# Kernel tuning notes

Measured on AMD Instinct MI355X. Metric: run time of the kernel, lower is better.

## Reference

```python
import jax, jax.numpy as jnp
import numpy as np

NUM_CODES = 100000
DIM = 64
N = 65536   # B*T flattened visits
L = 48      # max codes per visit (padded with -1)
C = 1.0     # Poincare ball curvature
MIN_NORM = 1e-15
BALL_EPS = 1e-5   # geoopt projx boundary eps for float32
ATANH_EPS = 1e-7  # clamp artanh argument below 1


def _projx(x):
    # Poincare ball projection: pull points with norm >= (1-eps)/sqrt(c) back inside.
    sqrt_c = jnp.sqrt(C)
    norm = jnp.maximum(jnp.linalg.norm(x, axis=-1, keepdims=True), MIN_NORM)
    maxnorm = (1.0 - BALL_EPS) / sqrt_c
    return jnp.where(norm > maxnorm, x * (maxnorm / norm), x)


def setup_inputs() -> dict:
    key = jax.random.key(0)
    k1, k2, k3 = jax.random.split(key, 3)
    emb = jax.random.normal(k1, (NUM_CODES, DIM), dtype=jnp.float32) * 0.001
    emb = _projx(emb)
    ids = jax.random.randint(k2, (N, L), 0, NUM_CODES)
    pad = jax.random.uniform(k3, (N, L)) < 0.3
    code_ids = jnp.where(pad, jnp.int64(-1) if jax.config.jax_enable_x64 else -1, ids)
    return {"code_ids": code_ids, "emb": emb}


def reference(code_ids, emb):
    # code_ids: [N, L] int, -1 = padding; emb: [NUM_CODES, DIM] Poincare points.
    sqrt_c = jnp.sqrt(jnp.asarray(C, emb.dtype))
    mask = code_ids >= 0                               # [N, L]
    safe_ids = jnp.where(mask, code_ids, 0)
    x = emb[safe_ids]                                  # [N, L, D] gather
    # logmap0: artanh(sqrt(c)*||x||) * x / (sqrt(c)*||x||)
    norm = jnp.maximum(jnp.linalg.norm(x, axis=-1, keepdims=True), MIN_NORM)
    arg = jnp.minimum(sqrt_c * norm, 1.0 - ATANH_EPS)
    tangents = (jnp.arctanh(arg) / (sqrt_c * norm)) * x  # [N, L, D]
    m = mask[..., None].astype(emb.dtype)
    s = jnp.sum(tangents * m, axis=1)                  # [N, D]
    cnt = jnp.sum(m, axis=1)                           # [N, 1]
    return s / jnp.maximum(cnt, 1.0)                   # zeros for empty visits
```

## Files before the change

kernel.cpp:

```cpp
#include <hip/hip_runtime.h>


#define LCODES 48
#define DIM 64

__global__ __launch_bounds__(256)
void amax_kernel(const float* __restrict__ emb, unsigned* __restrict__ bmax,
                 long n4) {
    const uint4* __restrict__ u4 = reinterpret_cast<const uint4*>(emb);
    unsigned m = 0;
    for (long i = (long)blockIdx.x * 256 + threadIdx.x; i < n4; i += 256L * 256L) {
        const uint4 w = u4[i];
        m = max(m, w.x & 0x7fffffffu);
        m = max(m, w.y & 0x7fffffffu);
        m = max(m, w.z & 0x7fffffffu);
        m = max(m, w.w & 0x7fffffffu);
    }
    #pragma unroll
    for (int d = 1; d <= 32; d <<= 1)
        m = max(m, (unsigned)__shfl_xor((int)m, d, 64));
    __shared__ unsigned sm[4];
    if ((threadIdx.x & 63) == 0) sm[threadIdx.x >> 6] = m;
    __syncthreads();
    if (threadIdx.x == 0)
        bmax[blockIdx.x] = max(max(sm[0], sm[1]), max(sm[2], sm[3]));
}

__device__ __forceinline__ float global_amax(const unsigned* __restrict__ bmax) {
    const int lane = threadIdx.x & 63;
    unsigned m = max(max(bmax[lane], bmax[lane + 64]),
                     max(bmax[lane + 128], bmax[lane + 192]));
    #pragma unroll
    for (int d = 1; d <= 32; d <<= 1)
        m = max(m, (unsigned)__shfl_xor((int)m, d, 64));
    return __uint_as_float(m);
}

__global__ __launch_bounds__(256)
void build_i8_kernel(const float* __restrict__ emb,
                     const unsigned* __restrict__ bmax,
                     unsigned char* __restrict__ tab,
                     float* __restrict__ qsout, int C) {
    const float amax = global_amax(bmax);
    const float qs   = amax * (1.0006f / 127.f);
    const float invq = (amax > 0.f) ? (127.f / (amax * 1.0006f)) : 0.f;
    if (blockIdx.x == 0 && threadIdx.x == 0) qsout[0] = qs;

    const int tid  = threadIdx.x;
    const int lane = tid & 63;
    const int wave = tid >> 6;
    const int g = lane >> 3;
    const int s = lane & 7;
    const int r = blockIdx.x * 32 + wave * 8 + g;
    if (r >= C) return;

    const float4* __restrict__ emb4 = reinterpret_cast<const float4*>(emb);
    const float4 a = emb4[r * 16 + 2 * s];
    const float4 b = emb4[r * 16 + 2 * s + 1];

    float ss = a.x*a.x + a.y*a.y + a.z*a.z + a.w*a.w
             + b.x*b.x + b.y*b.y + b.z*b.z + b.w*b.w;
    ss += __shfl_xor(ss, 1, 64);
    ss += __shfl_xor(ss, 2, 64);
    ss += __shfl_xor(ss, 4, 64);

    float scale;
    if (__builtin_expect(ss > 0.04f, 0)) {
        const float norm = fmaxf(sqrtf(ss), 1e-15f);
        const float arg  = fminf(norm, 1.f - 1e-7f);
        scale = 0.5f * logf((1.f + arg) / (1.f - arg)) / norm;
    } else {
        scale = 1.f + ss * (0.33333333333f + ss * (0.2f + ss * 0.14285714285f));
    }
    scale *= invq;

    const float t[8] = { a.x*scale, a.y*scale, a.z*scale, a.w*scale,
                         b.x*scale, b.y*scale, b.z*scale, b.w*scale };
    unsigned u[8];
    #pragma unroll
    for (int k = 0; k < 8; ++k)
        u[k] = (unsigned)((int)rintf(t[k]) + 128);

    uint2 w;
    w.x = u[0] | (u[1] << 8) | (u[2] << 16) | (u[3] << 24);
    w.y = u[4] | (u[5] << 8) | (u[6] << 16) | (u[7] << 24);
    reinterpret_cast<uint2*>(tab)[r * 8 + s] = w;
}

__global__ __launch_bounds__(256)
void visit_gather_i8_kernel(const int* __restrict__ ids,
                            const unsigned char* __restrict__ tab,
                            const float* __restrict__ qsp,
                            float* __restrict__ out, int N) {
    const float qs = qsp[0];

    const int tid  = threadIdx.x;
    const int lane = tid & 63;
    const int wave = tid >> 6;
    const int v    = blockIdx.x * 4 + wave;
    if (v >= N) return;

    int myid = -1;
    if (lane < LCODES) myid = ids[(long)v * LCODES + lane];

    const unsigned long long valid = __ballot(myid >= 0);
    const float cnt = (float)__popcll(valid);

    const int g = lane >> 3;
    const int s = lane & 7;

    const uint2* __restrict__ tab2 = reinterpret_cast<const uint2*>(tab);

    float4 accA = make_float4(0.f, 0.f, 0.f, 0.f);
    float4 accB = make_float4(0.f, 0.f, 0.f, 0.f);

    #pragma unroll
    for (int it = 0; it < LCODES / 8; ++it) {
        const int id     = __shfl(myid, it * 8 + g, 64);
        const float keep = (id >= 0) ? 1.f : 0.f;
        const unsigned base = ((unsigned)(id >= 0 ? id : 0)) << 3;

        const uint2 w = tab2[base + s];

        accA.x += (float)( w.x        & 0xff) * keep;
        accA.y += (float)((w.x >>  8) & 0xff) * keep;
        accA.z += (float)((w.x >> 16) & 0xff) * keep;
        accA.w += (float)( w.x >> 24        ) * keep;
        accB.x += (float)( w.y        & 0xff) * keep;
        accB.y += (float)((w.y >>  8) & 0xff) * keep;
        accB.z += (float)((w.y >> 16) & 0xff) * keep;
        accB.w += (float)( w.y >> 24        ) * keep;
    }

    #pragma unroll
    for (int d = 8; d <= 32; d <<= 1) {
        accA.x += __shfl_xor(accA.x, d, 64);
        accA.y += __shfl_xor(accA.y, d, 64);
        accA.z += __shfl_xor(accA.z, d, 64);
        accA.w += __shfl_xor(accA.w, d, 64);
        accB.x += __shfl_xor(accB.x, d, 64);
        accB.y += __shfl_xor(accB.y, d, 64);
        accB.z += __shfl_xor(accB.z, d, 64);
        accB.w += __shfl_xor(accB.w, d, 64);
    }

    if (lane < 8) {
        const float inv  = 1.f / fmaxf(cnt, 1.f);
        const float bias = 128.f * cnt;
        float4 rA = make_float4(qs * (accA.x - bias) * inv, qs * (accA.y - bias) * inv,
                                qs * (accA.z - bias) * inv, qs * (accA.w - bias) * inv);
        float4 rB = make_float4(qs * (accB.x - bias) * inv, qs * (accB.y - bias) * inv,
                                qs * (accB.z - bias) * inv, qs * (accB.w - bias) * inv);
        float4* o = reinterpret_cast<float4*>(out) + (long)v * (DIM / 4);
        o[2 * s]     = rA;
        o[2 * s + 1] = rB;
    }
}

__global__ __launch_bounds__(256, 4)
void visit_fp32_kernel(const int* __restrict__ ids,
                       const float* __restrict__ emb,
                       float* __restrict__ out, int N) {
    const int tid  = threadIdx.x;
    const int lane = tid & 63;
    const int wave = tid >> 6;
    const int v    = blockIdx.x * 4 + wave;
    if (v >= N) return;

    int myid = -1;
    if (lane < LCODES) myid = ids[(long)v * LCODES + lane];
    const unsigned long long valid = __ballot(myid >= 0);
    const float cnt = (float)__popcll(valid);
    const int g = lane >> 3, s = lane & 7;
    const float4* __restrict__ emb4 = reinterpret_cast<const float4*>(emb);
    float4 accA = make_float4(0.f,0.f,0.f,0.f), accB = make_float4(0.f,0.f,0.f,0.f);
    #pragma unroll
    for (int it = 0; it < LCODES / 8; ++it) {
        const int id = __shfl(myid, it * 8 + g, 64);
        const float keep = (id >= 0) ? 1.f : 0.f;
        const unsigned base = ((unsigned)(id >= 0 ? id : 0)) << 4;
        float4 a = emb4[base + s], b = emb4[base + 8 + s];
        float ss = a.x*a.x + a.y*a.y + a.z*a.z + a.w*a.w
                 + b.x*b.x + b.y*b.y + b.z*b.z + b.w*b.w;
        ss += __shfl_xor(ss, 1, 64);
        ss += __shfl_xor(ss, 2, 64);
        ss += __shfl_xor(ss, 4, 64);
        float scale;
        if (__builtin_expect(__any(ss > 0.04f), 0)) {
            const float norm = fmaxf(sqrtf(ss), 1e-15f);
            const float arg  = fminf(norm, 1.f - 1e-7f);
            scale = 0.5f * logf((1.f + arg) / (1.f - arg)) / norm;
        } else {
            scale = 1.f + ss * (0.33333333333f + ss * (0.2f + ss * 0.14285714285f));
        }
        scale *= keep;
        accA.x += a.x*scale; accA.y += a.y*scale; accA.z += a.z*scale; accA.w += a.w*scale;
        accB.x += b.x*scale; accB.y += b.y*scale; accB.z += b.z*scale; accB.w += b.w*scale;
    }
    #pragma unroll
    for (int d = 8; d <= 32; d <<= 1) {
        accA.x += __shfl_xor(accA.x, d, 64); accA.y += __shfl_xor(accA.y, d, 64);
        accA.z += __shfl_xor(accA.z, d, 64); accA.w += __shfl_xor(accA.w, d, 64);
        accB.x += __shfl_xor(accB.x, d, 64); accB.y += __shfl_xor(accB.y, d, 64);
        accB.z += __shfl_xor(accB.z, d, 64); accB.w += __shfl_xor(accB.w, d, 64);
    }
    if (lane < 8) {
        const float inv = 1.f / fmaxf(cnt, 1.f);
        float4* o = reinterpret_cast<float4*>(out) + (long)v * (DIM / 4);
        o[2*s]   = make_float4(accA.x*inv, accA.y*inv, accA.z*inv, accA.w*inv);
        o[2*s+1] = make_float4(accB.x*inv, accB.y*inv, accB.z*inv, accB.w*inv);
    }
}

extern "C" void kernel_launch(void* const* d_in, const int* in_sizes, int n_in,
                              void* d_out, int out_size, void* d_ws, size_t ws_size,
                              hipStream_t stream) {
    const int*   ids = (const int*)d_in[0];
    const float* emb = (const float*)d_in[1];
    float*       out = (float*)d_out;

    const int N = in_sizes[0] / LCODES;
    const int C = in_sizes[1] / DIM;

    const size_t tab_off = 4096;
    const size_t need = tab_off + (size_t)C * DIM;

    if (ws_size >= need) {
        unsigned*      bmax = (unsigned*)d_ws;
        float*         qsp  = (float*)((char*)d_ws + 1024);
        unsigned char* tab  = (unsigned char*)d_ws + tab_off;

        const long n4 = (long)C * DIM / 4;
        hipLaunchKernelGGL(amax_kernel, dim3(256), dim3(256), 0, stream,
                           emb, bmax, n4);
        const int blocksA = (C + 31) / 32;
        hipLaunchKernelGGL(build_i8_kernel, dim3(blocksA), dim3(256), 0, stream,
                           emb, bmax, tab, qsp, C);
        const int blocksB = (N + 3) / 4;
        hipLaunchKernelGGL(visit_gather_i8_kernel, dim3(blocksB), dim3(256), 0, stream,
                           ids, tab, qsp, out, N);
    } else {
        const int blocks = (N + 3) / 4;
        hipLaunchKernelGGL(visit_fp32_kernel, dim3(blocks), dim3(256), 0, stream,
                           ids, emb, out, N);
    }
}
```

Measured before the change: 110.8 us.

## Fuse amax, int8 table build and gather into one cooperative kernel

Replaces the three-kernel sequence (amax reduction, int8 table build, visit gather) with a single cooperative grid-stride kernel of 2048 blocks that uses grid.sync between phases. This removes two kernel launch gaps. The gather accumulation also switches from per-byte float adds to packed 16-bit integer SIMD-within-a-register adds on the masked words, which cuts the ALU work per loaded word. Costs are the grid-wide barriers, a fixed grid size that may limit occupancy during the gather phase, and a fallback to the old path if the cooperative launch fails.

New measurement: 426.3 us. 285% more time.

```diff
diff --git a/kernel.cpp b/kernel.cpp
--- a/kernel.cpp
+++ b/kernel.cpp
@@ -1,8 +1,162 @@
 #include <hip/hip_runtime.h>
+#include <hip/hip_cooperative_groups.h>
+
+namespace cg = cooperative_groups;
 
 
 #define LCODES 48
 #define DIM 64
+#define NBLK 2048
+#define NTHR 256
+
+__global__ __launch_bounds__(NTHR, 8)
+void fused_kernel(const int* __restrict__ ids,
+                  const float* __restrict__ emb,
+                  unsigned char* __restrict__ tab,
+                  unsigned* __restrict__ bmax,
+                  float* __restrict__ out,
+                  int N, int C) {
+    cg::grid_group grid = cg::this_grid();
+    const int tid  = threadIdx.x;
+    const int lane = tid & 63;
+    const int wave = tid >> 6;
+    const int bid  = blockIdx.x;
+
+    __shared__ unsigned sm[4];
+
+    {
+        const long n4 = (long)C * DIM / 4;
+        const uint4* __restrict__ u4 = reinterpret_cast<const uint4*>(emb);
+        unsigned m = 0;
+        for (long i = (long)bid * NTHR + tid; i < n4; i += (long)NBLK * NTHR) {
+            const uint4 w = u4[i];
+            m = max(m, w.x & 0x7fffffffu);
+            m = max(m, w.y & 0x7fffffffu);
+            m = max(m, w.z & 0x7fffffffu);
+            m = max(m, w.w & 0x7fffffffu);
+        }
+        #pragma unroll
+        for (int d = 1; d <= 32; d <<= 1)
+            m = max(m, (unsigned)__shfl_xor((int)m, d, 64));
+        if (lane == 0) sm[wave] = m;
+        __syncthreads();
+        if (tid == 0) bmax[bid] = max(max(sm[0], sm[1]), max(sm[2], sm[3]));
+    }
+    grid.sync();
+
+    float qs, invq;
+    {
+        unsigned gm = 0;
+        for (int i = tid; i < NBLK; i += NTHR) gm = max(gm, bmax[i]);
+        #pragma unroll
+        for (int d = 1; d <= 32; d <<= 1)
+            gm = max(gm, (unsigned)__shfl_xor((int)gm, d, 64));
+        __syncthreads();
+        if (lane == 0) sm[wave] = gm;
+        __syncthreads();
+        const unsigned g0 = max(max(sm[0], sm[1]), max(sm[2], sm[3]));
+        const float amax = __uint_as_float(g0);
+        qs   = amax * (1.0006f / 127.f);
+        invq = (amax > 0.f) ? (127.f / (amax * 1.0006f)) : 0.f;
+    }
+    {
+        const int g = lane >> 3;
+        const int s = lane & 7;
+        const float4* __restrict__ emb4 = reinterpret_cast<const float4*>(emb);
+        for (int rb = bid * 32; rb < C; rb += NBLK * 32) {
+            const int r = rb + wave * 8 + g;
+            if (r < C) {
+                const float4 a = emb4[r * 16 + 2 * s];
+                const float4 b = emb4[r * 16 + 2 * s + 1];
+
+                float ss = a.x*a.x + a.y*a.y + a.z*a.z + a.w*a.w
+                         + b.x*b.x + b.y*b.y + b.z*b.z + b.w*b.w;
+                ss += __shfl_xor(ss, 1, 64);
+                ss += __shfl_xor(ss, 2, 64);
+                ss += __shfl_xor(ss, 4, 64);
+
+                float scale;
+                if (__builtin_expect(ss > 0.04f, 0)) {
+                    const float norm = fmaxf(sqrtf(ss), 1e-15f);
+                    const float arg  = fminf(norm, 1.f - 1e-7f);
+                    scale = 0.5f * logf((1.f + arg) / (1.f - arg)) / norm;
+                } else {
+                    scale = 1.f + ss * (0.33333333333f + ss * (0.2f + ss * 0.14285714285f));
+                }
+                scale *= invq;
+
+                const float t[8] = { a.x*scale, a.y*scale, a.z*scale, a.w*scale,
+                                     b.x*scale, b.y*scale, b.z*scale, b.w*scale };
+                unsigned u[8];
+                #pragma unroll
+                for (int k = 0; k < 8; ++k)
+                    u[k] = (unsigned)((int)rintf(t[k]) + 128);
+
+                uint2 w;
+                w.x = u[0] | (u[1] << 8) | (u[2] << 16) | (u[3] << 24);
+                w.y = u[4] | (u[5] << 8) | (u[6] << 16) | (u[7] << 24);
+                reinterpret_cast<uint2*>(tab)[r * 8 + s] = w;
+            }
+        }
+    }
+    grid.sync();
+
+    {
+        const int g = lane >> 3;
+        const int s = lane & 7;
+        const uint2* __restrict__ tab2 = reinterpret_cast<const uint2*>(tab);
+
+        for (int v = bid * 4 + wave; v < N; v += NBLK * 4) {
+            int myid = -1;
+            if (lane < LCODES) myid = ids[(long)v * LCODES + lane];
+
+            const unsigned long long valid = __ballot(myid >= 0);
+            const float cnt = (float)__popcll(valid);
+
+            unsigned aEx = 0, aOx = 0, aEy = 0, aOy = 0;
+
+            #pragma unroll
+            for (int it = 0; it < LCODES / 8; ++it) {
+                const int id = __shfl(myid, it * 8 + g, 64);
+                const unsigned msk  = (id >= 0) ? 0xffffffffu : 0u;
+                const unsigned base = ((unsigned)(id >= 0 ? id : 0)) << 3;
+
+                uint2 w = tab2[base + s];
+                w.x &= msk;  w.y &= msk;
+
+                aEx +=  w.x       & 0x00ff00ffu;
+                aOx += (w.x >> 8) & 0x00ff00ffu;
+                aEy +=  w.y       & 0x00ff00ffu;
+                aOy += (w.y >> 8) & 0x00ff00ffu;
+            }
+
+            #pragma unroll
+            for (int d = 8; d <= 32; d <<= 1) {
+                aEx += (unsigned)__shfl_xor((int)aEx, d, 64);
+                aOx += (unsigned)__shfl_xor((int)aOx, d, 64);
+                aEy += (unsigned)__shfl_xor((int)aEy, d, 64);
+                aOy += (unsigned)__shfl_xor((int)aOy, d, 64);
+            }
+
+            if (lane < 8) {
+                const float qinv  = qs / fmaxf(cnt, 1.f);
+                const float fbias = 128.f * cnt;
+                float4 rA, rB;
+                rA.x = ((float)(aEx & 0xffffu) - fbias) * qinv;
+                rA.y = ((float)(aOx & 0xffffu) - fbias) * qinv;
+                rA.z = ((float)(aEx >> 16)     - fbias) * qinv;
+                rA.w = ((float)(aOx >> 16)     - fbias) * qinv;
+                rB.x = ((float)(aEy & 0xffffu) - fbias) * qinv;
+                rB.y = ((float)(aOy & 0xffffu) - fbias) * qinv;
+                rB.z = ((float)(aEy >> 16)     - fbias) * qinv;
+                rB.w = ((float)(aOy >> 16)     - fbias) * qinv;
+                float4* o = reinterpret_cast<float4*>(out) + (long)v * (DIM / 4);
+                o[2 * s]     = rA;
+                o[2 * s + 1] = rB;
+            }
+        }
+    }
+}
 
 __global__ __launch_bounds__(256)
 void amax_kernel(const float* __restrict__ emb, unsigned* __restrict__ bmax,
@@ -26,7 +180,7 @@
         bmax[blockIdx.x] = max(max(sm[0], sm[1]), max(sm[2], sm[3]));
 }
 
-__device__ __forceinline__ float global_amax(const unsigned* __restrict__ bmax) {
+__device__ __forceinline__ float global_amax256(const unsigned* __restrict__ bmax) {
     const int lane = threadIdx.x & 63;
     unsigned m = max(max(bmax[lane], bmax[lane + 64]),
                      max(bmax[lane + 128], bmax[lane + 192]));
@@ -41,7 +195,7 @@
                      const unsigned* __restrict__ bmax,
                      unsigned char* __restrict__ tab,
                      float* __restrict__ qsout, int C) {
-    const float amax = global_amax(bmax);
+    const float amax = global_amax256(bmax);
     const float qs   = amax * (1.0006f / 127.f);
     const float invq = (amax > 0.f) ? (127.f / (amax * 1.0006f)) : 0.f;
     if (blockIdx.x == 0 && threadIdx.x == 0) qsout[0] = qs;
@@ -49,8 +203,7 @@
     const int tid  = threadIdx.x;
     const int lane = tid & 63;
     const int wave = tid >> 6;
-    const int g = lane >> 3;
-    const int s = lane & 7;
+    const int g = lane >> 3, s = lane & 7;
     const int r = blockIdx.x * 32 + wave * 8 + g;
     if (r >= C) return;
 
@@ -93,7 +246,6 @@
                             const float* __restrict__ qsp,
                             float* __restrict__ out, int N) {
     const float qs = qsp[0];
-
     const int tid  = threadIdx.x;
     const int lane = tid & 63;
     const int wave = tid >> 6;
@@ -102,55 +254,43 @@
 
     int myid = -1;
     if (lane < LCODES) myid = ids[(long)v * LCODES + lane];
-
     const unsigned long long valid = __ballot(myid >= 0);
     const float cnt = (float)__popcll(valid);
-
-    const int g = lane >> 3;
-    const int s = lane & 7;
-
+    const int g = lane >> 3, s = lane & 7;
     const uint2* __restrict__ tab2 = reinterpret_cast<const uint2*>(tab);
 
-    float4 accA = make_float4(0.f, 0.f, 0.f, 0.f);
-    float4 accB = make_float4(0.f, 0.f, 0.f, 0.f);
-
+    unsigned aEx = 0, aOx = 0, aEy = 0, aOy = 0;
     #pragma unroll
     for (int it = 0; it < LCODES / 8; ++it) {
-        const int id     = __shfl(myid, it * 8 + g, 64);
-        const float keep = (id >= 0) ? 1.f : 0.f;
+        const int id = __shfl(myid, it * 8 + g, 64);
+        const unsigned msk  = (id >= 0) ? 0xffffffffu : 0u;
         const unsigned base = ((unsigned)(id >= 0 ? id : 0)) << 3;
-
-        const uint2 w = tab2[base + s];
-
-        accA.x += (float)( w.x        & 0xff) * keep;
-        accA.y += (float)((w.x >>  8) & 0xff) * keep;
-        accA.z += (float)((w.x >> 16) & 0xff) * keep;
-        accA.w += (float)( w.x >> 24        ) * keep;
-        accB.x += (float)( w.y        & 0xff) * keep;
-        accB.y += (float)((w.y >>  8) & 0xff) * keep;
-        accB.z += (float)((w.y >> 16) & 0xff) * keep;
-        accB.w += (float)( w.y >> 24        ) * keep;
-    }
-
+        uint2 w = tab2[base + s];
+        w.x &= msk;  w.y &= msk;
+        aEx +=  w.x       & 0x00ff00ffu;
+        aOx += (w.x >> 8) & 0x00ff00ffu;
+        aEy +=  w.y       & 0x00ff00ffu;
+        aOy += (w.y >> 8) & 0x00ff00ffu;
+    }
     #pragma unroll
     for (int d = 8; d <= 32; d <<= 1) {
-        accA.x += __shfl_xor(accA.x, d, 64);
-        accA.y += __shfl_xor(accA.y, d, 64);
-        accA.z += __shfl_xor(accA.z, d, 64);
-        accA.w += __shfl_xor(accA.w, d, 64);
-        accB.x += __shfl_xor(accB.x, d, 64);
-        accB.y += __shfl_xor(accB.y, d, 64);
-        accB.z += __shfl_xor(accB.z, d, 64);
-        accB.w += __shfl_xor(accB.w, d, 64);
-    }
-
+        aEx += (unsigned)__shfl_xor((int)aEx, d, 64);
+        aOx += (unsigned)__shfl_xor((int)aOx, d, 64);
+        aEy += (unsigned)__shfl_xor((int)aEy, d, 64);
+        aOy += (unsigned)__shfl_xor((int)aOy, d, 64);
+    }
     if (lane < 8) {
-        const float inv  = 1.f / fmaxf(cnt, 1.f);
-        const float bias = 128.f * cnt;
-        float4 rA = make_float4(qs * (accA.x - bias) * inv, qs * (accA.y - bias) * inv,
-                                qs * (accA.z - bias) * inv, qs * (accA.w - bias) * inv);
-        float4 rB = make_float4(qs * (accB.x - bias) * inv, qs * (accB.y - bias) * inv,
-                                qs * (accB.z - bias) * inv, qs * (accB.w - bias) * inv);
+        const float qinv  = qs / fmaxf(cnt, 1.f);
+        const float fbias = 128.f * cnt;
+        float4 rA, rB;
+        rA.x = ((float)(aEx & 0xffffu) - fbias) * qinv;
+        rA.y = ((float)(aOx & 0xffffu) - fbias) * qinv;
+        rA.z = ((float)(aEx >> 16)     - fbias) * qinv;
+        rA.w = ((float)(aOx >> 16)     - fbias) * qinv;
+        rB.x = ((float)(aEy & 0xffffu) - fbias) * qinv;
+        rB.y = ((float)(aOy & 0xffffu) - fbias) * qinv;
+        rB.z = ((float)(aEy >> 16)     - fbias) * qinv;
+        rB.w = ((float)(aOy >> 16)     - fbias) * qinv;
         float4* o = reinterpret_cast<float4*>(out) + (long)v * (DIM / 4);
         o[2 * s]     = rA;
         o[2 * s + 1] = rB;
@@ -222,23 +362,31 @@
     const int N = in_sizes[0] / LCODES;
     const int C = in_sizes[1] / DIM;
 
-    const size_t tab_off = 4096;
+    const size_t tab_off = 16384;
     const size_t need = tab_off + (size_t)C * DIM;
 
     if (ws_size >= need) {
         unsigned*      bmax = (unsigned*)d_ws;
-        float*         qsp  = (float*)((char*)d_ws + 1024);
+        float*         qsp  = (float*)((char*)d_ws + 8192);
         unsigned char* tab  = (unsigned char*)d_ws + tab_off;
 
-        const long n4 = (long)C * DIM / 4;
-        hipLaunchKernelGGL(amax_kernel, dim3(256), dim3(256), 0, stream,
-                           emb, bmax, n4);
-        const int blocksA = (C + 31) / 32;
-        hipLaunchKernelGGL(build_i8_kernel, dim3(blocksA), dim3(256), 0, stream,
-                           emb, bmax, tab, qsp, C);
-        const int blocksB = (N + 3) / 4;
-        hipLaunchKernelGGL(visit_gather_i8_kernel, dim3(blocksB), dim3(256), 0, stream,
-                           ids, tab, qsp, out, N);
+        int n = N, c = C;
+        void* args[] = { (void*)&ids, (void*)&emb, (void*)&tab,
+                         (void*)&bmax, (void*)&out, (void*)&n, (void*)&c };
+        hipError_t err = hipLaunchCooperativeKernel(
+            (void*)fused_kernel, dim3(NBLK), dim3(NTHR), args, 0, stream);
+
+        if (err != hipSuccess) {
+            const long n4 = (long)C * DIM / 4;
+            hipLaunchKernelGGL(amax_kernel, dim3(256), dim3(256), 0, stream,
+                               emb, bmax, n4);
+            const int blocksA = (C + 31) / 32;
+            hipLaunchKernelGGL(build_i8_kernel, dim3(blocksA), dim3(256), 0, stream,
+                               emb, bmax, tab, qsp, C);
+            const int blocksB = (N + 3) / 4;
+            hipLaunchKernelGGL(visit_gather_i8_kernel, dim3(blocksB), dim3(256), 0,
+                               stream, ids, tab, qsp, out, N);
+        }
     } else {
         const int blocks = (N + 3) / 4;
         hipLaunchKernelGGL(visit_fp32_kernel, dim3(blocks), dim3(256), 0, stream,
```

## Process two visits per wave with packed 16-bit SWAR integer accumulation

Applied to the files above, without the earlier changes.

Each wave in the gather kernel now handles two visits, so it issues twice as many independent table loads per iteration. Accumulation switches from eight float adds per load to packed-integer SWAR sums, with two byte lanes held in 16-bit halves of each register. The shuffle reduction also runs on the packed integers, roughly halving the shuffle count per visit. Headroom holds: 48 codes times 255 fits in 16 bits, but register pressure and write divergence rise somewhat.

Measured after the change: 107.9 us. 2.6% less time.

```diff
diff --git a/kernel.cpp b/kernel.cpp
--- a/kernel.cpp
+++ b/kernel.cpp
@@ -26,7 +26,7 @@
         bmax[blockIdx.x] = max(max(sm[0], sm[1]), max(sm[2], sm[3]));
 }
 
-__device__ __forceinline__ float global_amax(const unsigned* __restrict__ bmax) {
+__device__ __forceinline__ float global_amax256(const unsigned* __restrict__ bmax) {
     const int lane = threadIdx.x & 63;
     unsigned m = max(max(bmax[lane], bmax[lane + 64]),
                      max(bmax[lane + 128], bmax[lane + 192]));
@@ -41,7 +41,7 @@
                      const unsigned* __restrict__ bmax,
                      unsigned char* __restrict__ tab,
                      float* __restrict__ qsout, int C) {
-    const float amax = global_amax(bmax);
+    const float amax = global_amax256(bmax);
     const float qs   = amax * (1.0006f / 127.f);
     const float invq = (amax > 0.f) ? (127.f / (amax * 1.0006f)) : 0.f;
     if (blockIdx.x == 0 && threadIdx.x == 0) qsout[0] = qs;
@@ -49,8 +49,7 @@
     const int tid  = threadIdx.x;
     const int lane = tid & 63;
     const int wave = tid >> 6;
-    const int g = lane >> 3;
-    const int s = lane & 7;
+    const int g = lane >> 3, s = lane & 7;
     const int r = blockIdx.x * 32 + wave * 8 + g;
     if (r >= C) return;
 
@@ -88,72 +87,98 @@
 }
 
 __global__ __launch_bounds__(256)
-void visit_gather_i8_kernel(const int* __restrict__ ids,
-                            const unsigned char* __restrict__ tab,
-                            const float* __restrict__ qsp,
-                            float* __restrict__ out, int N) {
+void visit_gather_i8x2_kernel(const int* __restrict__ ids,
+                              const unsigned char* __restrict__ tab,
+                              const float* __restrict__ qsp,
+                              float* __restrict__ out, int N) {
     const float qs = qsp[0];
 
     const int tid  = threadIdx.x;
     const int lane = tid & 63;
     const int wave = tid >> 6;
-    const int v    = blockIdx.x * 4 + wave;
-    if (v >= N) return;
-
-    int myid = -1;
-    if (lane < LCODES) myid = ids[(long)v * LCODES + lane];
-
-    const unsigned long long valid = __ballot(myid >= 0);
-    const float cnt = (float)__popcll(valid);
+    const int v0   = (blockIdx.x * 4 + wave) * 2;
+    if (v0 >= N) return;
+    const bool has1 = (v0 + 1) < N;
+
+    int myid0 = -1, myid1 = -1;
+    if (lane < LCODES) {
+        myid0 = ids[(long)v0 * LCODES + lane];
+        if (has1) myid1 = ids[(long)(v0 + 1) * LCODES + lane];
+    }
+
+    const float cnt0 = (float)__popcll(__ballot(myid0 >= 0));
+    const float cnt1 = (float)__popcll(__ballot(myid1 >= 0));
 
     const int g = lane >> 3;
     const int s = lane & 7;
-
     const uint2* __restrict__ tab2 = reinterpret_cast<const uint2*>(tab);
 
-    float4 accA = make_float4(0.f, 0.f, 0.f, 0.f);
-    float4 accB = make_float4(0.f, 0.f, 0.f, 0.f);
+    unsigned aEx0 = 0, aOx0 = 0, aEy0 = 0, aOy0 = 0;
+    unsigned aEx1 = 0, aOx1 = 0, aEy1 = 0, aOy1 = 0;
 
     #pragma unroll
     for (int it = 0; it < LCODES / 8; ++it) {
-        const int id     = __shfl(myid, it * 8 + g, 64);
-        const float keep = (id >= 0) ? 1.f : 0.f;
-        const unsigned base = ((unsigned)(id >= 0 ? id : 0)) << 3;
-
-        const uint2 w = tab2[base + s];
-
-        accA.x += (float)( w.x        & 0xff) * keep;
-        accA.y += (float)((w.x >>  8) & 0xff) * keep;
-        accA.z += (float)((w.x >> 16) & 0xff) * keep;
-        accA.w += (float)( w.x >> 24        ) * keep;
-        accB.x += (float)( w.y        & 0xff) * keep;
-        accB.y += (float)((w.y >>  8) & 0xff) * keep;
-        accB.z += (float)((w.y >> 16) & 0xff) * keep;
-        accB.w += (float)( w.y >> 24        ) * keep;
+        const int j   = it * 8 + g;
+        const int id0 = __shfl(myid0, j, 64);
+        const int id1 = __shfl(myid1, j, 64);
+        const unsigned msk0  = (id0 >= 0) ? 0xffffffffu : 0u;
+        const unsigned msk1  = (id1 >= 0) ? 0xffffffffu : 0u;
+        const unsigned base0 = ((unsigned)(id0 >= 0 ? id0 : 0)) << 3;
+        const unsigned base1 = ((unsigned)(id1 >= 0 ? id1 : 0)) << 3;
+
+        uint2 w0 = tab2[base0 + s];
+        uint2 w1 = tab2[base1 + s];
+        w0.x &= msk0;  w0.y &= msk0;
+        w1.x &= msk1;  w1.y &= msk1;
+
+        aEx0 +=  w0.x       & 0x00ff00ffu;
+        aOx0 += (w0.x >> 8) & 0x00ff00ffu;
+        aEy0 +=  w0.y       & 0x00ff00ffu;
+        aOy0 += (w0.y >> 8) & 0x00ff00ffu;
+        aEx1 +=  w1.x       & 0x00ff00ffu;
+        aOx1 += (w1.x >> 8) & 0x00ff00ffu;
+        aEy1 +=  w1.y       & 0x00ff00ffu;
+        aOy1 += (w1.y >> 8) & 0x00ff00ffu;
     }
 
     #pragma unroll
     for (int d = 8; d <= 32; d <<= 1) {
-        accA.x += __shfl_xor(accA.x, d, 64);
-        accA.y += __shfl_xor(accA.y, d, 64);
-        accA.z += __shfl_xor(accA.z, d, 64);
-        accA.w += __shfl_xor(accA.w, d, 64);
-        accB.x += __shfl_xor(accB.x, d, 64);
-        accB.y += __shfl_xor(accB.y, d, 64);
-        accB.z += __shfl_xor(accB.z, d, 64);
-        accB.w += __shfl_xor(accB.w, d, 64);
-    }
-
-    if (lane < 8) {
-        const float inv  = 1.f / fmaxf(cnt, 1.f);
-        const float bias = 128.f * cnt;
-        float4 rA = make_float4(qs * (accA.x - bias) * inv, qs * (accA.y - bias) * inv,
-                                qs * (accA.z - bias) * inv, qs * (accA.w - bias) * inv);
-        float4 rB = make_float4(qs * (accB.x - bias) * inv, qs * (accB.y - bias) * inv,
-                                qs * (accB.z - bias) * inv, qs * (accB.w - bias) * inv);
-        float4* o = reinterpret_cast<float4*>(out) + (long)v * (DIM / 4);
-        o[2 * s]     = rA;
-        o[2 * s + 1] = rB;
+        aEx0 += (unsigned)__shfl_xor((int)aEx0, d, 64);
+        aOx0 += (unsigned)__shfl_xor((int)aOx0, d, 64);
+        aEy0 += (unsigned)__shfl_xor((int)aEy0, d, 64);
+        aOy0 += (unsigned)__shfl_xor((int)aOy0, d, 64);
+        aEx1 += (unsigned)__shfl_xor((int)aEx1, d, 64);
+        aOx1 += (unsigned)__shfl_xor((int)aOx1, d, 64);
+        aEy1 += (unsigned)__shfl_xor((int)aEy1, d, 64);
+        aOy1 += (unsigned)__shfl_xor((int)aOy1, d, 64);
+    }
+
+    if (lane < 16) {
+        const bool second = lane >= 8;
+        if (!second || has1) {
+            const int  ss8   = lane & 7;
+            const int  v     = v0 + (second ? 1 : 0);
+            const float cnt  = second ? cnt1 : cnt0;
+            const unsigned eX = second ? aEx1 : aEx0;
+            const unsigned oX = second ? aOx1 : aOx0;
+            const unsigned eY = second ? aEy1 : aEy0;
+            const unsigned oY = second ? aOy1 : aOy0;
+
+            const float qinv  = qs / fmaxf(cnt, 1.f);
+            const float fbias = 128.f * cnt;
+            float4 rA, rB;
+            rA.x = ((float)(eX & 0xffffu) - fbias) * qinv;
+            rA.y = ((float)(oX & 0xffffu) - fbias) * qinv;
+            rA.z = ((float)(eX >> 16)     - fbias) * qinv;
+            rA.w = ((float)(oX >> 16)     - fbias) * qinv;
+            rB.x = ((float)(eY & 0xffffu) - fbias) * qinv;
+            rB.y = ((float)(oY & 0xffffu) - fbias) * qinv;
+            rB.z = ((float)(eY >> 16)     - fbias) * qinv;
+            rB.w = ((float)(oY >> 16)     - fbias) * qinv;
+            float4* o = reinterpret_cast<float4*>(out) + (long)v * (DIM / 4);
+            o[2 * ss8]     = rA;
+            o[2 * ss8 + 1] = rB;
+        }
     }
 }
 
@@ -236,9 +261,9 @@
         const int blocksA = (C + 31) / 32;
         hipLaunchKernelGGL(build_i8_kernel, dim3(blocksA), dim3(256), 0, stream,
                            emb, bmax, tab, qsp, C);
-        const int blocksB = (N + 3) / 4;
-        hipLaunchKernelGGL(visit_gather_i8_kernel, dim3(blocksB), dim3(256), 0, stream,
-                           ids, tab, qsp, out, N);
+        const int blocksB = (N + 7) / 8;
+        hipLaunchKernelGGL(visit_gather_i8x2_kernel, dim3(blocksB), dim3(256), 0,
+                           stream, ids, tab, qsp, out, N);
     } else {
         const int blocks = (N + 3) / 4;
         hipLaunchKernelGGL(visit_fp32_kernel, dim3(blocks), dim3(256), 0, stream,
```
